# Performance work log

Measured on AMD Instinct MI355X. Metric: run time of the kernel, lower is better.

The kernel has to match this reference:

```python
import jax, jax.numpy as jnp
import numpy as np

N = 16384          # tokens
D_IN = 512         # input_dim
D_OUT = 512        # output_dim
H = 256            # expert hidden
E = 10             # num_experts
TOP_K = 2


def setup_inputs() -> dict:
    key = jax.random.key(0)
    ks = jax.random.split(key, 12)
    s_in = 1.0 / np.sqrt(D_IN)
    s_h = 1.0 / np.sqrt(H)
    s_o = 1.0 / np.sqrt(D_OUT)
    return {
        "x": jax.random.normal(ks[0], (N, D_IN), dtype=jnp.float32),
        "gate_w": jax.random.uniform(ks[1], (D_IN, E), minval=-s_in, maxval=s_in),
        "gate_b": jax.random.uniform(ks[2], (E,), minval=-s_in, maxval=s_in),
        "w1": jax.random.uniform(ks[3], (E, D_IN, H), minval=-s_in, maxval=s_in),
        "b1": jax.random.uniform(ks[4], (E, H), minval=-s_in, maxval=s_in),
        "w2": jax.random.uniform(ks[5], (E, H, D_OUT), minval=-s_h, maxval=s_h),
        "b2": jax.random.uniform(ks[6], (E, D_OUT), minval=-s_h, maxval=s_h),
        "cls_w": jax.random.uniform(ks[7], (D_OUT, D_OUT), minval=-s_o, maxval=s_o),
        "cls_b": jax.random.uniform(ks[8], (D_OUT,), minval=-s_o, maxval=s_o),
        "vec_w": jax.random.uniform(ks[9], (D_OUT, D_OUT), minval=-s_o, maxval=s_o),
        "vec_b": jax.random.uniform(ks[10], (D_OUT,), minval=-s_o, maxval=s_o),
    }


def reference(x, gate_w, gate_b, w1, b1, w2, b2, cls_w, cls_b, vec_w, vec_b):
    # Gating: softmax over experts, take top-k, renormalize
    gate_probs = jax.nn.softmax(x @ gate_w + gate_b, axis=-1)          # [N, E]
    top_v, top_i = jax.lax.top_k(gate_probs, TOP_K)                    # [N, K]
    top_v = top_v / jnp.sum(top_v, axis=-1, keepdims=True)
    # Scatter renormalized top-k probs into dense per-expert weights [N, E]
    n_idx = jnp.arange(x.shape[0])[:, None]
    w = jnp.zeros_like(gate_probs).at[n_idx, top_i].add(top_v)
    # Expert MLPs (vectorized over experts; zero weight == not dispatched)
    h = jax.nn.relu(jnp.einsum("nd,edh->neh", x, w1) + b1)             # [N, E, H]
    y = jnp.einsum("neh,eho->neo", h, w2) + b2                          # [N, E, Dout]
    combined = jnp.einsum("neo,ne->no", y, w)                           # [N, Dout]
    cls_out = combined @ cls_w + cls_b
    vec_out = combined @ vec_w + vec_b
    return (cls_out, vec_out)
```

## Files before the change

### kernel.cpp

```cpp
#include <hip/hip_runtime.h>

#define NTOK 16384
#define DIN  512
#define DOUT 512
#define HDIM 256
#define NEXP 10
#define NSLOT (2*NTOK)
#define NSEG  (2*NEXP)
#define BM 128
#define BN 128
#define BK 64

typedef unsigned short u16;
typedef unsigned int   u32;
typedef short s16x8 __attribute__((ext_vector_type(8)));
typedef float f32x4 __attribute__((ext_vector_type(4)));

__device__ __forceinline__ u16 f2b(float f){
  union { float f; u32 u; } c; c.f = f;
  u32 r = c.u + 0x7FFFu + ((c.u >> 16) & 1u);
  return (u16)(r >> 16);
}
__device__ __forceinline__ float b2f(u16 v){
  union { u32 u; float f; } c; c.u = ((u32)v) << 16; return c.f;
}
__device__ __forceinline__ u32 pk2(float lo, float hi){
  u32 r;
  asm("v_cvt_pk_bf16_f32 %0, %1, %2" : "=v"(r) : "v"(lo), "v"(hi));
  return r;
}
__device__ __forceinline__ s16x8 cvt8(const float* p){
  f32x4 a = *(const f32x4*)p;
  f32x4 b = *(const f32x4*)(p + 4);
  union { u32 u[4]; s16x8 v; } c;
  c.u[0] = pk2(a[0], a[1]); c.u[1] = pk2(a[2], a[3]);
  c.u[2] = pk2(b[0], b[1]); c.u[3] = pk2(b[2], b[3]);
  return c.v;
}

__global__ __launch_bounds__(64) void k_zero(int* counts){
  if (threadIdx.x < NSEG) counts[threadIdx.x] = 0;
}

__global__ __launch_bounds__(256) void k_gate(
    const float* __restrict__ x, const float* __restrict__ gw, const float* __restrict__ gb,
    int* __restrict__ tke, float* __restrict__ tkw, int* __restrict__ counts)
{
  __shared__ int cnt[NSEG];
  __shared__ __align__(16) float xs[16*512];
  __shared__ __align__(16) float lgw[5120];
  const int tid = threadIdx.x;
  if (tid < NSEG) cnt[tid] = 0;
  for (int d = tid; d < 512; d += 256){
    float g[10];
    #pragma unroll
    for (int r = 0; r < 10; ++r) g[r] = gw[d*10 + r];
    #pragma unroll
    for (int p = 0; p < 5; ++p){
      lgw[(p*512 + d)*2    ] = g[2*p];
      lgw[(p*512 + d)*2 + 1] = g[2*p+1];
    }
  }
  const float* xsrc = x + (size_t)blockIdx.x * 16 * 512;
  #pragma unroll
  for (int q = 0; q < 8; ++q){
    int i = tid + q*256;
    *(f32x4*)&xs[i*4] = *(const f32x4*)&xsrc[i*4];
  }
  __syncthreads();

  const int wave = tid >> 6, lane = tid & 63;
  #pragma unroll
  for (int tt = 0; tt < 4; ++tt){
    const int lt = wave*4 + tt;
    const int token = blockIdx.x*16 + lt;
    float acc[NEXP];
    #pragma unroll
    for (int e = 0; e < NEXP; ++e) acc[e] = 0.f;
    #pragma unroll
    for (int dd = 0; dd < 8; ++dd){
      int d = dd*64 + lane;
      float xv = xs[lt*512 + d];
      #pragma unroll
      for (int p = 0; p < 5; ++p){
        float2 g2 = *(const float2*)&lgw[(p*512 + d)*2];
        acc[2*p]   += xv * g2.x;
        acc[2*p+1] += xv * g2.y;
      }
    }
    #pragma unroll
    for (int e = 0; e < NEXP; ++e){
      #pragma unroll
      for (int off = 32; off > 0; off >>= 1) acc[e] += __shfl_xor(acc[e], off, 64);
    }
    if (lane == 0){
      float l[NEXP];
      #pragma unroll
      for (int e = 0; e < NEXP; ++e) l[e] = acc[e] + gb[e];
      int bi = 0; float bv = l[0];
      #pragma unroll
      for (int e = 1; e < NEXP; ++e) if (l[e] > bv){ bv = l[e]; bi = e; }
      int si = -1; float sv = -1e30f;
      #pragma unroll
      for (int e = 0; e < NEXP; ++e) if (e != bi && l[e] > sv){ sv = l[e]; si = e; }
      float w0 = 1.f / (1.f + expf(sv - bv));
      tke[2*token]   = bi;  tke[2*token+1] = si;
      tkw[2*token]   = w0;  tkw[2*token+1] = 1.f - w0;
      atomicAdd(&cnt[2*bi], 1);  atomicAdd(&cnt[2*si+1], 1);
    }
  }
  __syncthreads();
  if (tid < NSEG && cnt[tid] > 0)
    atomicAdd(&counts[tid], cnt[tid]);
}

__global__ __launch_bounds__(64) void k_scan(
    const int* __restrict__ counts, int* __restrict__ offsets, int* __restrict__ cursors)
{
  if (threadIdx.x == 0){
    int s = 0;
    for (int i = 0; i < NSEG; ++i){ offsets[i] = s; s += counts[i]; }
    offsets[NSEG] = s;
  }
  if (threadIdx.x < NSEG) cursors[threadIdx.x] = 0;
}

__global__ __launch_bounds__(256) void k_scatter(
    const int* __restrict__ tke, const float* __restrict__ tkw,
    const int* __restrict__ offsets, int* __restrict__ cursors,
    int* __restrict__ tok_slot, float* __restrict__ w_slot)
{
  __shared__ int lcnt[NSEG], lbase[NSEG];
  if (threadIdx.x < NSEG) lcnt[threadIdx.x] = 0;
  __syncthreads();
  int n = blockIdx.x * 256 + threadIdx.x;
  int g0 = 2*tke[2*n], g1 = 2*tke[2*n+1] + 1;
  int p0 = atomicAdd(&lcnt[g0], 1);
  int p1 = atomicAdd(&lcnt[g1], 1);
  __syncthreads();
  if (threadIdx.x < NSEG) lbase[threadIdx.x] = atomicAdd(&cursors[threadIdx.x], lcnt[threadIdx.x]);
  __syncthreads();
  int s0 = offsets[g0] + lbase[g0] + p0;
  int s1 = offsets[g1] + lbase[g1] + p1;
  tok_slot[s0] = n; w_slot[s0] = tkw[2*n];
  tok_slot[s1] = n; w_slot[s1] = tkw[2*n+1];
}

__global__ __launch_bounds__(256) void k_wtf(
    const float* __restrict__ W, u16* __restrict__ out, int KC8, int C16)
{
  const int e   = blockIdx.z;
  const int gid = blockIdx.x * 256 + threadIdx.x;
  const int c16 = gid & 15;
  const int rem = gid >> 4;
  const int kc  = rem % KC8;
  const int cg  = rem / KC8;
  const int K = KC8 * 8, C = C16 * 16;
  const float* src = W + (size_t)e*K*C + (size_t)(kc*8)*C + cg*16 + c16;
  s16x8 v;
  #pragma unroll
  for (int q = 0; q < 8; ++q)
    v[q] = (short)f2b(src[(size_t)q * C]);
  size_t t = ((size_t)e*C16 + cg)*KC8 + kc;
  *(s16x8*)(out + t*128 + c16*8) = v;
}

__global__ __launch_bounds__(256, 3) void k_h(
    const float* __restrict__ x, const u16* __restrict__ w1f, const float* __restrict__ b1,
    const int* __restrict__ offsets, const int* __restrict__ tok_slot,
    u16* __restrict__ h)
{
  __shared__ __align__(16) char pool[34816];
  u16* As = (u16*)pool;
  __shared__ int toks[BM];
  const int e   = blockIdx.z;
  const int hh  = blockIdx.y;
  const int off = offsets[2*e];
  const int cnt = offsets[2*e+2] - off;
  const int c0  = blockIdx.x * BM;
  if (c0 >= cnt) return;
  const int tid = threadIdx.x;

  if (tid < BM){
    int r = c0 + tid;
    toks[tid] = tok_slot[off + (r < cnt ? r : cnt - 1)];
  }
  __syncthreads();

  int crow[4], ckk[4];
  #pragma unroll
  for (int i = 0; i < 4; ++i){
    int c = tid + i*256;
    crow[i] = c >> 3; ckk[i] = (c & 7) * 8;
  }
  int tokr[4];
  #pragma unroll
  for (int i = 0; i < 4; ++i) tokr[i] = toks[crow[i]];

  s16x8 ra[4];
  auto loadregs = [&](int ks){
    #pragma unroll
    for (int i = 0; i < 4; ++i)
      ra[i] = cvt8(x + (size_t)tokr[i]*DIN + ks*BK + ckk[i]);
  };
  auto writeregs = [&](int buf){
    #pragma unroll
    for (int i = 0; i < 4; ++i){
      u32 byt = (u32)((crow[i]*BK + ckk[i])*2) ^ ((u32)(crow[i]&7)<<4);
      *(s16x8*)((char*)As + buf*16384 + byt) = ra[i];
    }
  };

  const int wv = tid >> 6, lane = tid & 63;
  const int lr = lane & 15, lk = lane >> 4;
  const int wr = (wv >> 1) * 64, wc = (wv & 1) * 64;
  const int cgb = e*16 + hh*8 + (wv & 1)*4;

  f32x4 acc[4][4];
  #pragma unroll
  for (int i = 0; i < 4; ++i)
    #pragma unroll
    for (int j = 0; j < 4; ++j) acc[i][j] = (f32x4){0.f,0.f,0.f,0.f};

  loadregs(0); writeregs(0);
  int cur = 0;
  const int NK = DIN / BK;
  for (int ks = 0; ks < NK; ++ks){
    __syncthreads();
    if (ks + 1 < NK) loadregs(ks + 1);
    #pragma unroll
    for (int sub = 0; sub < 2; ++sub){
      int kc = ks*8 + sub*4 + lk;
      s16x8 af[4], bf[4];
      #pragma unroll
      for (int g = 0; g < 4; ++g){
        int arow = wr + g*16 + lr;
        u32 ab = (u32)((arow*BK + sub*32 + lk*8)*2) ^ ((u32)(arow&7)<<4);
        af[g] = *(const s16x8*)((char*)As + cur*16384 + ab);
        bf[g] = *(const s16x8*)(w1f + ((size_t)(cgb + g)*64 + kc)*128 + lr*8);
      }
      #pragma unroll
      for (int i = 0; i < 4; ++i)
        #pragma unroll
        for (int j = 0; j < 4; ++j)
          acc[i][j] = __builtin_amdgcn_mfma_f32_16x16x32_bf16(af[i], bf[j], acc[i][j], 0, 0, 0);
    }
    if (ks + 1 < NK) writeregs(cur ^ 1);
    cur ^= 1;
  }
  __syncthreads();

  u16* outh = (u16*)pool;
  const int n0 = hh * 128;
  #pragma unroll
  for (int j = 0; j < 4; ++j){
    int col = wc + j*16 + lr;
    float bias = b1[e*HDIM + n0 + col];
    #pragma unroll
    for (int i = 0; i < 4; ++i)
      #pragma unroll
      for (int r = 0; r < 4; ++r){
        int row = wr + i*16 + lk*4 + r;
        float v = acc[i][j][r] + bias;
        outh[row*136 + col] = f2b(v > 0.f ? v : 0.f);
      }
  }
  __syncthreads();
  {
    int r = tid >> 1, half = tid & 1;
    if (c0 + r < cnt){
      u16* dst = h + (size_t)(off + c0 + r) * HDIM + n0 + half*64;
      const u16* src = outh + r*136 + half*64;
      #pragma unroll
      for (int q = 0; q < 8; ++q)
        *(s16x8*)(dst + q*8) = *(const s16x8*)(src + q*8);
    }
  }
}

template<int PASS>
__global__ __launch_bounds__(256, 3) void k_y(
    const u16* __restrict__ h, const u16* __restrict__ w2f, const float* __restrict__ b2,
    const int* __restrict__ offsets, const int* __restrict__ tok_slot,
    const float* __restrict__ w_slot, u16* __restrict__ cmb)
{
  __shared__ __align__(16) char pool[34816];
  u16* As = (u16*)pool;
  __shared__ int   toks[BM];
  __shared__ float wts[BM];
  const int e    = blockIdx.z;
  const int q4   = blockIdx.y;
  const int segb = offsets[2*e + PASS];
  const int segc = offsets[2*e + PASS + 1] - segb;
  const int c0   = blockIdx.x * BM;
  if (c0 >= segc) return;
  const int n0   = q4 * BN;
  const int tid  = threadIdx.x;

  if (tid < BM){
    int r = c0 + tid;
    int s = segb + (r < segc ? r : segc - 1);
    toks[tid] = tok_slot[s];
    wts[tid]  = w_slot[s];
  }
  __syncthreads();

  const u16* Ag = h + (size_t)(segb + c0) * HDIM;

  int crow[4], ckk[4];
  #pragma unroll
  for (int i = 0; i < 4; ++i){
    int c = tid + i*256;
    crow[i] = c >> 3; ckk[i] = (c & 7) * 8;
  }
  s16x8 ra[4];
  auto loadregs = [&](int ks){
    #pragma unroll
    for (int i = 0; i < 4; ++i)
      ra[i] = *(const s16x8*)(Ag + (size_t)crow[i]*HDIM + ks*BK + ckk[i]);
  };
  auto writeregs = [&](int buf){
    #pragma unroll
    for (int i = 0; i < 4; ++i){
      u32 byt = (u32)((crow[i]*BK + ckk[i])*2) ^ ((u32)(crow[i]&7)<<4);
      *(s16x8*)((char*)As + buf*16384 + byt) = ra[i];
    }
  };

  const int wv = tid >> 6, lane = tid & 63;
  const int lr = lane & 15, lk = lane >> 4;
  const int wr = (wv >> 1) * 64, wc = (wv & 1) * 64;
  const int cgb = e*32 + q4*8 + (wv & 1)*4;

  f32x4 acc[4][4];
  #pragma unroll
  for (int i = 0; i < 4; ++i)
    #pragma unroll
    for (int j = 0; j < 4; ++j) acc[i][j] = (f32x4){0.f,0.f,0.f,0.f};

  loadregs(0); writeregs(0);
  int cur = 0;
  const int NK = HDIM / BK;
  for (int ks = 0; ks < NK; ++ks){
    __syncthreads();
    if (ks + 1 < NK) loadregs(ks + 1);
    #pragma unroll
    for (int sub = 0; sub < 2; ++sub){
      int kc = ks*8 + sub*4 + lk;
      s16x8 af[4], bf[4];
      #pragma unroll
      for (int g = 0; g < 4; ++g){
        int arow = wr + g*16 + lr;
        u32 ab = (u32)((arow*BK + sub*32 + lk*8)*2) ^ ((u32)(arow&7)<<4);
        af[g] = *(const s16x8*)((char*)As + cur*16384 + ab);
        bf[g] = *(const s16x8*)(w2f + ((size_t)(cgb + g)*32 + kc)*128 + lr*8);
      }
      #pragma unroll
      for (int i = 0; i < 4; ++i)
        #pragma unroll
        for (int j = 0; j < 4; ++j)
          acc[i][j] = __builtin_amdgcn_mfma_f32_16x16x32_bf16(af[i], bf[j], acc[i][j], 0, 0, 0);
    }
    if (ks + 1 < NK) writeregs(cur ^ 1);
    cur ^= 1;
  }
  __syncthreads();

  u16* outh = (u16*)pool;
  #pragma unroll
  for (int j = 0; j < 4; ++j){
    int col = wc + j*16 + lr;
    float bias = b2[e*DOUT + n0 + col];
    #pragma unroll
    for (int i = 0; i < 4; ++i)
      #pragma unroll
      for (int r = 0; r < 4; ++r){
        int row = wr + i*16 + lk*4 + r;
        outh[row*136 + col] = f2b(wts[row] * (acc[i][j][r] + bias));
      }
  }
  __syncthreads();
  {
    int r = tid >> 1, half = tid & 1;
    if (c0 + r < segc){
      u16* dst = cmb + (size_t)toks[r] * 1024 + n0 + half*64;
      const u16* src = outh + r*136 + half*64;
      #pragma unroll
      for (int q = 0; q < 8; ++q){
        s16x8 s = *(const s16x8*)(src + q*8);
        if (PASS == 1){
          s16x8 old = *(const s16x8*)(dst + q*8);
          #pragma unroll
          for (int m = 0; m < 8; ++m)
            s[m] = (short)f2b(b2f((u16)old[m]) + b2f((u16)s[m]));
        }
        *(s16x8*)(dst + q*8) = s;
      }
    }
  }
}

__global__ __launch_bounds__(512, 4) void k_cls(
    const u16* __restrict__ cmb, const float* __restrict__ W,
    const float* __restrict__ bias, float* __restrict__ out)
{
  __shared__ __align__(16) char Bs[2][10240];
  const int tid = threadIdx.x;
  const int r0  = blockIdx.x * 256;
  const int c0  = blockIdx.y * 128;

  const int bc4 = tid >> 4;
  const int bkp = tid & 15;
  u32 bpk[4];
  auto loadB = [&](int ks){
    const float* p0 = W + (size_t)(ks*32 + 2*bkp) * DOUT + c0 + bc4*4;
    f32x4 v0 = *(const f32x4*)p0;
    f32x4 v1 = *(const f32x4*)(p0 + DOUT);
    #pragma unroll
    for (int m = 0; m < 4; ++m) bpk[m] = pk2(v0[m], v1[m]);
  };
  auto writeB = [&](int buf){
    #pragma unroll
    for (int m = 0; m < 4; ++m)
      *(u32*)(Bs[buf] + (bc4*4 + m)*80 + bkp*4) = bpk[m];
  };

  const int wv = tid >> 6, lane = tid & 63;
  const int lr = lane & 15, lk = lane >> 4;
  const int rg = wv >> 1, cg = wv & 1;
  const u16* Arow = cmb + (size_t)(r0 + rg*64) * 1024;

  f32x4 acc[4][4];
  #pragma unroll
  for (int i = 0; i < 4; ++i)
    #pragma unroll
    for (int j = 0; j < 4; ++j) acc[i][j] = (f32x4){0.f,0.f,0.f,0.f};

  s16x8 af[4], afn[4];
  auto loadA = [&](s16x8* a, int ks){
    #pragma unroll
    for (int g = 0; g < 4; ++g)
      a[g] = *(const s16x8*)(Arow + (size_t)(g*16 + lr)*1024 + ks*32 + lk*8);
  };

  loadB(0); writeB(0); loadA(af, 0);
  int cur = 0;
  for (int ks = 0; ks < 16; ++ks){
    __syncthreads();
    if (ks + 1 < 16){ loadB(ks + 1); loadA(afn, ks + 1); }
    s16x8 bf[4];
    #pragma unroll
    for (int j = 0; j < 4; ++j)
      bf[j] = *(const s16x8*)(Bs[cur] + (cg*64 + j*16 + lr)*80 + lk*16);
    #pragma unroll
    for (int i = 0; i < 4; ++i)
      #pragma unroll
      for (int j = 0; j < 4; ++j)
        acc[i][j] = __builtin_amdgcn_mfma_f32_16x16x32_bf16(af[i], bf[j], acc[i][j], 0, 0, 0);
    if (ks + 1 < 16) writeB(cur ^ 1);
    #pragma unroll
    for (int g = 0; g < 4; ++g) af[g] = afn[g];
    cur ^= 1;
  }

  #pragma unroll
  for (int j = 0; j < 4; ++j){
    int col = c0 + cg*64 + j*16 + lr;
    float bv = bias[col];
    #pragma unroll
    for (int i = 0; i < 4; ++i)
      #pragma unroll
      for (int r = 0; r < 4; ++r){
        int row = r0 + rg*64 + i*16 + lk*4 + r;
        out[(size_t)row * DOUT + col] = acc[i][j][r] + bv;
      }
  }
}

__global__ __launch_bounds__(512, 2) void k_vip(
    const float* __restrict__ W, const float* __restrict__ bias,
    u16* __restrict__ cmbio)
{
  __shared__ __align__(16) char Bs[2][40960];
  const int tid = threadIdx.x;
  const int r0  = blockIdx.x * 64;

  int bc4[4], bkp[4];
  #pragma unroll
  for (int u = 0; u < 4; ++u){
    int idx = tid + u*512;
    bc4[u] = idx >> 4;
    bkp[u] = idx & 15;
  }
  u32 bpk[4][4];
  auto loadB = [&](int ks){
    #pragma unroll
    for (int u = 0; u < 4; ++u){
      const float* p0 = W + (size_t)(ks*32 + 2*bkp[u]) * DOUT + bc4[u]*4;
      f32x4 v0 = *(const f32x4*)p0;
      f32x4 v1 = *(const f32x4*)(p0 + DOUT);
      #pragma unroll
      for (int m = 0; m < 4; ++m) bpk[u][m] = pk2(v0[m], v1[m]);
    }
  };
  auto writeB = [&](int buf){
    #pragma unroll
    for (int u = 0; u < 4; ++u)
      #pragma unroll
      for (int m = 0; m < 4; ++m)
        *(u32*)(Bs[buf] + (bc4[u]*4 + m)*80 + bkp[u]*4) = bpk[u][m];
  };

  const int wv = tid >> 6, lane = tid & 63;
  const int lr = lane & 15, lk = lane >> 4;
  const int wc = wv * 64;
  const u16* Arow = cmbio + (size_t)r0 * 1024;

  f32x4 acc[4][4];
  #pragma unroll
  for (int i = 0; i < 4; ++i)
    #pragma unroll
    for (int j = 0; j < 4; ++j) acc[i][j] = (f32x4){0.f,0.f,0.f,0.f};

  s16x8 af[4], afn[4];
  auto loadA = [&](s16x8* a, int ks){
    #pragma unroll
    for (int g = 0; g < 4; ++g)
      a[g] = *(const s16x8*)(Arow + (size_t)(g*16 + lr)*1024 + ks*32 + lk*8);
  };

  loadB(0); writeB(0); loadA(af, 0);
  int cur = 0;
  for (int ks = 0; ks < 16; ++ks){
    __syncthreads();
    if (ks + 1 < 16){ loadB(ks + 1); loadA(afn, ks + 1); }
    s16x8 bf[4];
    #pragma unroll
    for (int g = 0; g < 4; ++g)
      bf[g] = *(const s16x8*)(Bs[cur] + (wc + g*16 + lr)*80 + lk*16);
    #pragma unroll
    for (int i = 0; i < 4; ++i)
      #pragma unroll
      for (int j = 0; j < 4; ++j)
        acc[i][j] = __builtin_amdgcn_mfma_f32_16x16x32_bf16(af[i], bf[j], acc[i][j], 0, 0, 0);
    if (ks + 1 < 16) writeB(cur ^ 1);
    #pragma unroll
    for (int g = 0; g < 4; ++g) af[g] = afn[g];
    cur ^= 1;
  }
  __syncthreads();

  float* out = (float*)cmbio;
  #pragma unroll
  for (int j = 0; j < 4; ++j){
    int col = wc + j*16 + lr;
    float bv = bias[col];
    #pragma unroll
    for (int i = 0; i < 4; ++i)
      #pragma unroll
      for (int r = 0; r < 4; ++r){
        int row = r0 + i*16 + lk*4 + r;
        out[(size_t)row * DOUT + col] = acc[i][j][r] + bv;
      }
  }
}

__global__ __launch_bounds__(256, 2) void k_vipw(
    const u16* __restrict__ wTt, const float* __restrict__ bias,
    u16* __restrict__ cmbio)
{
  const int tid = threadIdx.x;
  const int r0  = blockIdx.x * 32;
  const int wv = tid >> 6, lane = tid & 63;
  const int lr = lane & 15, lk = lane >> 4;
  const int wc = wv * 128;
  const int cg0 = wv * 8;
  const u16* Arow = cmbio + (size_t)r0 * 1024;

  f32x4 acc[2][8];
  #pragma unroll
  for (int i = 0; i < 2; ++i)
    #pragma unroll
    for (int j = 0; j < 8; ++j) acc[i][j] = (f32x4){0.f,0.f,0.f,0.f};

  s16x8 a0[2], b0[8], a1[2], b1[8];
  auto loadA = [&](s16x8* a, int ks){
    #pragma unroll
    for (int g = 0; g < 2; ++g)
      a[g] = *(const s16x8*)(Arow + (size_t)(g*16 + lr)*1024 + ks*32 + lk*8);
  };
  auto loadB = [&](s16x8* b, int ks){
    #pragma unroll
    for (int j = 0; j < 8; ++j){
      int chunk = (cg0 + j)*64 + ks*4 + lk;
      b[j] = *(const s16x8*)(wTt + (size_t)chunk*128 + lr*8);
    }
  };
  auto step = [&](const s16x8* a, const s16x8* b){
    #pragma unroll
    for (int j = 0; j < 8; ++j)
      #pragma unroll
      for (int i = 0; i < 2; ++i)
        acc[i][j] = __builtin_amdgcn_mfma_f32_16x16x32_bf16(a[i], b[j], acc[i][j], 0, 0, 0);
  };

  loadA(a0, 0); loadB(b0, 0);
  #pragma unroll
  for (int ks = 0; ks < 16; ks += 2){
    if (ks + 1 < 16){ loadA(a1, ks + 1); loadB(b1, ks + 1); }
    step(a0, b0);
    if (ks + 2 < 16){ loadA(a0, ks + 2); loadB(b0, ks + 2); }
    step(a1, b1);
  }
  __syncthreads();

  float* out = (float*)cmbio;
  #pragma unroll
  for (int j = 0; j < 8; ++j){
    int col = wc + j*16 + lr;
    float bv = bias[col];
    #pragma unroll
    for (int i = 0; i < 2; ++i)
      #pragma unroll
      for (int r = 0; r < 4; ++r){
        int row = r0 + i*16 + lk*4 + r;
        out[(size_t)row * DOUT + col] = acc[i][j][r] + bv;
      }
  }
}

extern "C" void kernel_launch(void* const* d_in, const int* in_sizes, int n_in,
                              void* d_out, int out_size, void* d_ws, size_t ws_size,
                              hipStream_t stream)
{
  const float* x    = (const float*)d_in[0];
  const float* gw   = (const float*)d_in[1];
  const float* gb   = (const float*)d_in[2];
  const float* w1   = (const float*)d_in[3];
  const float* b1   = (const float*)d_in[4];
  const float* w2   = (const float*)d_in[5];
  const float* b2   = (const float*)d_in[6];
  const float* clsw = (const float*)d_in[7];
  const float* clsb = (const float*)d_in[8];
  const float* vecw = (const float*)d_in[9];
  const float* vecb = (const float*)d_in[10];

  char* base = (char*)d_out;
  float* cls_out  = (float*)base;
  u16*   cmb      = (u16*)(base + ((size_t)32<<20));
  u16*   h        = (u16*)base;
  char*  mb       = base + ((size_t)16<<20) + (128<<10);
  int*   tok_slot = (int*)  mb;
  float* w_slot   = (float*)(mb + 131072);
  int*   tke      = (int*)  (mb + 262144);
  float* tkw      = (float*)(mb + 393216);
  int*   counts   = (int*)  (mb + 524288);
  int*   offsets  = (int*)  (mb + 524544);
  int*   cursors  = (int*)  (mb + 524800);
  u16*   w1f      = (u16*)(base + ((size_t)18<<20));
  u16*   w2f      = (u16*)(base + ((size_t)21<<20));

  const bool usews = (ws_size >= (size_t)(1<<20));
  u16* vecwTt = (u16*)d_ws;

  k_zero<<<dim3(1), dim3(64), 0, stream>>>(counts);
  k_gate<<<dim3(NTOK/16), dim3(256), 0, stream>>>(x, gw, gb, tke, tkw, counts);
  k_scan<<<dim3(1), dim3(64), 0, stream>>>(counts, offsets, cursors);
  k_scatter<<<dim3(NTOK/256), dim3(256), 0, stream>>>(tke, tkw, offsets, cursors,
                                                      tok_slot, w_slot);
  k_wtf<<<dim3(64, 1, NEXP), dim3(256), 0, stream>>>(w1, w1f, 64, 16);
  k_wtf<<<dim3(64, 1, NEXP), dim3(256), 0, stream>>>(w2, w2f, 32, 32);
  if (usews)
    k_wtf<<<dim3(128, 1, 1), dim3(256), 0, stream>>>(vecw, vecwTt, 64, 32);
  k_h<<<dim3(256, 2, NEXP), dim3(256), 0, stream>>>(x, w1f, b1, offsets, tok_slot, h);
  k_y<0><<<dim3(128, 4, NEXP), dim3(256), 0, stream>>>(h, w2f, b2, offsets, tok_slot, w_slot, cmb);
  k_y<1><<<dim3(128, 4, NEXP), dim3(256), 0, stream>>>(h, w2f, b2, offsets, tok_slot, w_slot, cmb);
  k_cls<<<dim3(NTOK/256, DOUT/128), dim3(512), 0, stream>>>(cmb, clsw, clsb, cls_out);
  if (usews)
    k_vipw<<<dim3(NTOK/32), dim3(256), 0, stream>>>(vecwTt, vecb, cmb);
  else
    k_vip<<<dim3(NTOK/64), dim3(512), 0, stream>>>(vecw, vecb, cmb);
}
```

Measured before the change: 203.7 us.

## Fuse expert up-projection and down-projection into one kernel keeping hidden in LDS

Replaces the separate k_h (x·W1 + relu to global h) and k_y (h·W2) kernels with a fused k_ey that computes a 64-token tile's hidden activations into shared memory and immediately multiplies by W2 for all 512 outputs. This removes the global round trip of the bf16 hidden buffer and one kernel launch. In exchange, each block now reads full W1 and W2 slices per 64 rows, and the fused kernel is run once per slot pass, so the up-projection on x is split across two launches. Both passes now recompute the gather and conversion of x. B operands still come straight from global memory, and each wave holds only one 16-row A fragment, which lowers MFMA reuse.

```diff
diff --git a/kernel.cpp b/kernel.cpp
--- a/kernel.cpp
+++ b/kernel.cpp
@@ -7,9 +7,6 @@
 #define NEXP 10
 #define NSLOT (2*NTOK)
 #define NSEG  (2*NEXP)
-#define BM 128
-#define BN 128
-#define BK 64
 
 typedef unsigned short u16;
 typedef unsigned int   u32;
@@ -165,139 +162,27 @@
   *(s16x8*)(out + t*128 + c16*8) = v;
 }
 
-__global__ __launch_bounds__(256, 3) void k_h(
-    const float* __restrict__ x, const u16* __restrict__ w1f, const float* __restrict__ b1,
-    const int* __restrict__ offsets, const int* __restrict__ tok_slot,
-    u16* __restrict__ h)
-{
-  __shared__ __align__(16) char pool[34816];
-  u16* As = (u16*)pool;
-  __shared__ int toks[BM];
-  const int e   = blockIdx.z;
-  const int hh  = blockIdx.y;
-  const int off = offsets[2*e];
-  const int cnt = offsets[2*e+2] - off;
-  const int c0  = blockIdx.x * BM;
-  if (c0 >= cnt) return;
-  const int tid = threadIdx.x;
-
-  if (tid < BM){
-    int r = c0 + tid;
-    toks[tid] = tok_slot[off + (r < cnt ? r : cnt - 1)];
-  }
-  __syncthreads();
-
-  int crow[4], ckk[4];
-  #pragma unroll
-  for (int i = 0; i < 4; ++i){
-    int c = tid + i*256;
-    crow[i] = c >> 3; ckk[i] = (c & 7) * 8;
-  }
-  int tokr[4];
-  #pragma unroll
-  for (int i = 0; i < 4; ++i) tokr[i] = toks[crow[i]];
-
-  s16x8 ra[4];
-  auto loadregs = [&](int ks){
-    #pragma unroll
-    for (int i = 0; i < 4; ++i)
-      ra[i] = cvt8(x + (size_t)tokr[i]*DIN + ks*BK + ckk[i]);
-  };
-  auto writeregs = [&](int buf){
-    #pragma unroll
-    for (int i = 0; i < 4; ++i){
-      u32 byt = (u32)((crow[i]*BK + ckk[i])*2) ^ ((u32)(crow[i]&7)<<4);
-      *(s16x8*)((char*)As + buf*16384 + byt) = ra[i];
-    }
-  };
-
-  const int wv = tid >> 6, lane = tid & 63;
-  const int lr = lane & 15, lk = lane >> 4;
-  const int wr = (wv >> 1) * 64, wc = (wv & 1) * 64;
-  const int cgb = e*16 + hh*8 + (wv & 1)*4;
-
-  f32x4 acc[4][4];
-  #pragma unroll
-  for (int i = 0; i < 4; ++i)
-    #pragma unroll
-    for (int j = 0; j < 4; ++j) acc[i][j] = (f32x4){0.f,0.f,0.f,0.f};
-
-  loadregs(0); writeregs(0);
-  int cur = 0;
-  const int NK = DIN / BK;
-  for (int ks = 0; ks < NK; ++ks){
-    __syncthreads();
-    if (ks + 1 < NK) loadregs(ks + 1);
-    #pragma unroll
-    for (int sub = 0; sub < 2; ++sub){
-      int kc = ks*8 + sub*4 + lk;
-      s16x8 af[4], bf[4];
-      #pragma unroll
-      for (int g = 0; g < 4; ++g){
-        int arow = wr + g*16 + lr;
-        u32 ab = (u32)((arow*BK + sub*32 + lk*8)*2) ^ ((u32)(arow&7)<<4);
-        af[g] = *(const s16x8*)((char*)As + cur*16384 + ab);
-        bf[g] = *(const s16x8*)(w1f + ((size_t)(cgb + g)*64 + kc)*128 + lr*8);
-      }
-      #pragma unroll
-      for (int i = 0; i < 4; ++i)
-        #pragma unroll
-        for (int j = 0; j < 4; ++j)
-          acc[i][j] = __builtin_amdgcn_mfma_f32_16x16x32_bf16(af[i], bf[j], acc[i][j], 0, 0, 0);
-    }
-    if (ks + 1 < NK) writeregs(cur ^ 1);
-    cur ^= 1;
-  }
-  __syncthreads();
-
-  u16* outh = (u16*)pool;
-  const int n0 = hh * 128;
-  #pragma unroll
-  for (int j = 0; j < 4; ++j){
-    int col = wc + j*16 + lr;
-    float bias = b1[e*HDIM + n0 + col];
-    #pragma unroll
-    for (int i = 0; i < 4; ++i)
-      #pragma unroll
-      for (int r = 0; r < 4; ++r){
-        int row = wr + i*16 + lk*4 + r;
-        float v = acc[i][j][r] + bias;
-        outh[row*136 + col] = f2b(v > 0.f ? v : 0.f);
-      }
-  }
-  __syncthreads();
-  {
-    int r = tid >> 1, half = tid & 1;
-    if (c0 + r < cnt){
-      u16* dst = h + (size_t)(off + c0 + r) * HDIM + n0 + half*64;
-      const u16* src = outh + r*136 + half*64;
-      #pragma unroll
-      for (int q = 0; q < 8; ++q)
-        *(s16x8*)(dst + q*8) = *(const s16x8*)(src + q*8);
-    }
-  }
-}
-
 template<int PASS>
-__global__ __launch_bounds__(256, 3) void k_y(
-    const u16* __restrict__ h, const u16* __restrict__ w2f, const float* __restrict__ b2,
+__global__ __launch_bounds__(512, 4) void k_ey(
+    const float* __restrict__ x,
+    const u16* __restrict__ w1f, const float* __restrict__ b1,
+    const u16* __restrict__ w2f, const float* __restrict__ b2,
     const int* __restrict__ offsets, const int* __restrict__ tok_slot,
     const float* __restrict__ w_slot, u16* __restrict__ cmb)
 {
-  __shared__ __align__(16) char pool[34816];
-  u16* As = (u16*)pool;
-  __shared__ int   toks[BM];
-  __shared__ float wts[BM];
+  __shared__ __align__(16) char pool[50176];
+  u16* As   = (u16*)pool;
+  u16* hbuf = (u16*)(pool + 16384);
+  __shared__ int   toks[64];
+  __shared__ float wts[64];
   const int e    = blockIdx.z;
-  const int q4   = blockIdx.y;
   const int segb = offsets[2*e + PASS];
   const int segc = offsets[2*e + PASS + 1] - segb;
-  const int c0   = blockIdx.x * BM;
+  const int c0   = blockIdx.x * 64;
   if (c0 >= segc) return;
-  const int n0   = q4 * BN;
   const int tid  = threadIdx.x;
 
-  if (tid < BM){
+  if (tid < 64){
     int r = c0 + tid;
     int s = segb + (r < segc ? r : segc - 1);
     toks[tid] = tok_slot[s];
@@ -305,98 +190,113 @@
   }
   __syncthreads();
 
-  const u16* Ag = h + (size_t)(segb + c0) * HDIM;
-
-  int crow[4], ckk[4];
-  #pragma unroll
-  for (int i = 0; i < 4; ++i){
-    int c = tid + i*256;
-    crow[i] = c >> 3; ckk[i] = (c & 7) * 8;
-  }
-  s16x8 ra[4];
+  const int crow = tid >> 3;
+  const int ckk  = (tid & 7) * 8;
+  const int tokr = toks[crow];
+
+  s16x8 ra;
   auto loadregs = [&](int ks){
-    #pragma unroll
-    for (int i = 0; i < 4; ++i)
-      ra[i] = *(const s16x8*)(Ag + (size_t)crow[i]*HDIM + ks*BK + ckk[i]);
+    ra = cvt8(x + (size_t)tokr*DIN + ks*64 + ckk);
   };
   auto writeregs = [&](int buf){
-    #pragma unroll
-    for (int i = 0; i < 4; ++i){
-      u32 byt = (u32)((crow[i]*BK + ckk[i])*2) ^ ((u32)(crow[i]&7)<<4);
-      *(s16x8*)((char*)As + buf*16384 + byt) = ra[i];
-    }
+    u32 byt = (u32)((crow*64 + ckk)*2) ^ ((u32)(crow&7)<<4);
+    *(s16x8*)((char*)As + buf*8192 + byt) = ra;
   };
 
   const int wv = tid >> 6, lane = tid & 63;
   const int lr = lane & 15, lk = lane >> 4;
-  const int wr = (wv >> 1) * 64, wc = (wv & 1) * 64;
-  const int cgb = e*32 + q4*8 + (wv & 1)*4;
-
-  f32x4 acc[4][4];
-  #pragma unroll
-  for (int i = 0; i < 4; ++i)
-    #pragma unroll
-    for (int j = 0; j < 4; ++j) acc[i][j] = (f32x4){0.f,0.f,0.f,0.f};
+  const int wr = (wv >> 1) * 16;
+  const int ch = wv & 1;
+
+  f32x4 acc1[8];
+  #pragma unroll
+  for (int j = 0; j < 8; ++j) acc1[j] = (f32x4){0.f,0.f,0.f,0.f};
+  const int cgb1 = e*16 + ch*8;
 
   loadregs(0); writeregs(0);
   int cur = 0;
-  const int NK = HDIM / BK;
-  for (int ks = 0; ks < NK; ++ks){
+  for (int ks = 0; ks < 8; ++ks){
     __syncthreads();
-    if (ks + 1 < NK) loadregs(ks + 1);
+    if (ks + 1 < 8) loadregs(ks + 1);
     #pragma unroll
     for (int sub = 0; sub < 2; ++sub){
       int kc = ks*8 + sub*4 + lk;
-      s16x8 af[4], bf[4];
-      #pragma unroll
-      for (int g = 0; g < 4; ++g){
-        int arow = wr + g*16 + lr;
-        u32 ab = (u32)((arow*BK + sub*32 + lk*8)*2) ^ ((u32)(arow&7)<<4);
-        af[g] = *(const s16x8*)((char*)As + cur*16384 + ab);
-        bf[g] = *(const s16x8*)(w2f + ((size_t)(cgb + g)*32 + kc)*128 + lr*8);
-      }
-      #pragma unroll
-      for (int i = 0; i < 4; ++i)
+      int arow = wr + lr;
+      u32 ab = (u32)((arow*64 + sub*32 + lk*8)*2) ^ ((u32)(arow&7)<<4);
+      s16x8 af = *(const s16x8*)((char*)As + cur*8192 + ab);
+      #pragma unroll
+      for (int g = 0; g < 8; ++g){
+        s16x8 bf = *(const s16x8*)(w1f + ((size_t)(cgb1 + g)*64 + kc)*128 + lr*8);
+        acc1[g] = __builtin_amdgcn_mfma_f32_16x16x32_bf16(af, bf, acc1[g], 0, 0, 0);
+      }
+    }
+    if (ks + 1 < 8) writeregs(cur ^ 1);
+    cur ^= 1;
+  }
+  #pragma unroll
+  for (int g = 0; g < 8; ++g){
+    int col = ch*128 + g*16 + lr;
+    float bias = b1[e*HDIM + col];
+    #pragma unroll
+    for (int r = 0; r < 4; ++r){
+      int row = wr + lk*4 + r;
+      float v = acc1[g][r] + bias;
+      hbuf[row*264 + col] = f2b(v > 0.f ? v : 0.f);
+    }
+  }
+  __syncthreads();
+
+  f32x4 acc2[16];
+  #pragma unroll
+  for (int g = 0; g < 16; ++g) acc2[g] = (f32x4){0.f,0.f,0.f,0.f};
+  const int cgb2 = e*32 + ch*16;
+
+  for (int kk = 0; kk < 8; ++kk){
+    s16x8 af = *(const s16x8*)&hbuf[(wr + lr)*264 + kk*32 + lk*8];
+    int kc = kk*4 + lk;
+    #pragma unroll
+    for (int g = 0; g < 16; ++g){
+      s16x8 bf = *(const s16x8*)(w2f + ((size_t)(cgb2 + g)*32 + kc)*128 + lr*8);
+      acc2[g] = __builtin_amdgcn_mfma_f32_16x16x32_bf16(af, bf, acc2[g], 0, 0, 0);
+    }
+  }
+  __syncthreads();
+
+  u16* stage = (u16*)pool;
+  #pragma unroll
+  for (int cc = 0; cc < 2; ++cc){
+    if (ch == cc){
+      #pragma unroll
+      for (int g = 0; g < 16; ++g){
+        int col = g*16 + lr;
+        float bias = b2[e*DOUT + cc*256 + col];
         #pragma unroll
-        for (int j = 0; j < 4; ++j)
-          acc[i][j] = __builtin_amdgcn_mfma_f32_16x16x32_bf16(af[i], bf[j], acc[i][j], 0, 0, 0);
-    }
-    if (ks + 1 < NK) writeregs(cur ^ 1);
-    cur ^= 1;
-  }
-  __syncthreads();
-
-  u16* outh = (u16*)pool;
-  #pragma unroll
-  for (int j = 0; j < 4; ++j){
-    int col = wc + j*16 + lr;
-    float bias = b2[e*DOUT + n0 + col];
-    #pragma unroll
-    for (int i = 0; i < 4; ++i)
-      #pragma unroll
-      for (int r = 0; r < 4; ++r){
-        int row = wr + i*16 + lk*4 + r;
-        outh[row*136 + col] = f2b(wts[row] * (acc[i][j][r] + bias));
-      }
-  }
-  __syncthreads();
-  {
-    int r = tid >> 1, half = tid & 1;
-    if (c0 + r < segc){
-      u16* dst = cmb + (size_t)toks[r] * 1024 + n0 + half*64;
-      const u16* src = outh + r*136 + half*64;
-      #pragma unroll
-      for (int q = 0; q < 8; ++q){
-        s16x8 s = *(const s16x8*)(src + q*8);
-        if (PASS == 1){
-          s16x8 old = *(const s16x8*)(dst + q*8);
-          #pragma unroll
-          for (int m = 0; m < 8; ++m)
-            s[m] = (short)f2b(b2f((u16)old[m]) + b2f((u16)s[m]));
+        for (int r = 0; r < 4; ++r){
+          int row = wr + lk*4 + r;
+          stage[row*264 + col] = f2b(wts[row] * (acc2[g][r] + bias));
         }
-        *(s16x8*)(dst + q*8) = s;
-      }
-    }
+      }
+    }
+    __syncthreads();
+    {
+      int row = tid >> 3, t8 = tid & 7;
+      if (c0 + row < segc){
+        u16* dst = cmb + (size_t)toks[row] * 1024 + cc*256 + t8*32;
+        const u16* src = stage + row*264 + t8*32;
+        #pragma unroll
+        for (int q = 0; q < 4; ++q){
+          s16x8 s = *(const s16x8*)(src + q*8);
+          if (PASS == 1){
+            s16x8 old = *(const s16x8*)(dst + q*8);
+            #pragma unroll
+            for (int m = 0; m < 8; ++m)
+              s[m] = (short)f2b(b2f((u16)old[m]) + b2f((u16)s[m]));
+          }
+          *(s16x8*)(dst + q*8) = s;
+        }
+      }
+    }
+    __syncthreads();
   }
 }
 
@@ -648,7 +548,6 @@
   char* base = (char*)d_out;
   float* cls_out  = (float*)base;
   u16*   cmb      = (u16*)(base + ((size_t)32<<20));
-  u16*   h        = (u16*)base;
   char*  mb       = base + ((size_t)16<<20) + (128<<10);
   int*   tok_slot = (int*)  mb;
   float* w_slot   = (float*)(mb + 131072);
@@ -672,9 +571,10 @@
   k_wtf<<<dim3(64, 1, NEXP), dim3(256), 0, stream>>>(w2, w2f, 32, 32);
   if (usews)
     k_wtf<<<dim3(128, 1, 1), dim3(256), 0, stream>>>(vecw, vecwTt, 64, 32);
-  k_h<<<dim3(256, 2, NEXP), dim3(256), 0, stream>>>(x, w1f, b1, offsets, tok_slot, h);
-  k_y<0><<<dim3(128, 4, NEXP), dim3(256), 0, stream>>>(h, w2f, b2, offsets, tok_slot, w_slot, cmb);
-  k_y<1><<<dim3(128, 4, NEXP), dim3(256), 0, stream>>>(h, w2f, b2, offsets, tok_slot, w_slot, cmb);
+  k_ey<0><<<dim3(256, 1, NEXP), dim3(512), 0, stream>>>(x, w1f, b1, w2f, b2,
+                                                        offsets, tok_slot, w_slot, cmb);
+  k_ey<1><<<dim3(256, 1, NEXP), dim3(512), 0, stream>>>(x, w1f, b1, w2f, b2,
+                                                        offsets, tok_slot, w_slot, cmb);
   k_cls<<<dim3(NTOK/256, DOUT/128), dim3(512), 0, stream>>>(cmb, clsw, clsb, cls_out);
   if (usews)
     k_vipw<<<dim3(NTOK/32), dim3(256), 0, stream>>>(vecwTt, vecb, cmb);
```

After: 283.0 us. 38.9% more time.

## Pre-pack cls weights to bf16 fragments and drop LDS staging in cls GEMM

Applied to the files above, without the earlier changes.

Adds a kernel that converts cls_w to bf16 in MFMA fragment order and stores it in the otherwise unused upper half of the first rows of the combined buffer. The classifier GEMM is rewritten so each block handles 32 rows across all 512 output columns, reading pre-packed B fragments straight from global memory with register double-buffering instead of converting fp32 weights into shared memory with barriers each k-step. This removes per-block weight conversion and LDS syncs, but relies on the spare region of cmb staying untouched until k_cls2 runs, and it leans on cache for the B reloads.

```diff
diff --git a/kernel.cpp b/kernel.cpp
--- a/kernel.cpp
+++ b/kernel.cpp
@@ -163,6 +163,24 @@
     v[q] = (short)f2b(src[(size_t)q * C]);
   size_t t = ((size_t)e*C16 + cg)*KC8 + kc;
   *(s16x8*)(out + t*128 + c16*8) = v;
+}
+
+__global__ __launch_bounds__(256) void k_wtc(
+    const float* __restrict__ W, u16* __restrict__ cmb)
+{
+  const int gid = blockIdx.x * 256 + threadIdx.x;
+  const int c16 = gid & 15;
+  const int rem = gid >> 4;
+  const int kc  = rem % 64;
+  const int cg  = rem / 64;
+  const float* src = W + (size_t)(kc*8)*DOUT + cg*16 + c16;
+  s16x8 v;
+  #pragma unroll
+  for (int q = 0; q < 8; ++q)
+    v[q] = (short)f2b(src[(size_t)q * DOUT]);
+  size_t t = (size_t)cg*64 + kc;
+  u16* dst = cmb + (t>>2)*1024 + 512 + (t&3)*128 + c16*8;
+  *(s16x8*)dst = v;
 }
 
 __global__ __launch_bounds__(256, 3) void k_h(
@@ -400,78 +418,63 @@
   }
 }
 
-__global__ __launch_bounds__(512, 4) void k_cls(
-    const u16* __restrict__ cmb, const float* __restrict__ W,
-    const float* __restrict__ bias, float* __restrict__ out)
-{
-  __shared__ __align__(16) char Bs[2][10240];
+__global__ __launch_bounds__(256, 2) void k_cls2(
+    const u16* __restrict__ cmb, const float* __restrict__ bias,
+    float* __restrict__ out)
+{
   const int tid = threadIdx.x;
-  const int r0  = blockIdx.x * 256;
-  const int c0  = blockIdx.y * 128;
-
-  const int bc4 = tid >> 4;
-  const int bkp = tid & 15;
-  u32 bpk[4];
-  auto loadB = [&](int ks){
-    const float* p0 = W + (size_t)(ks*32 + 2*bkp) * DOUT + c0 + bc4*4;
-    f32x4 v0 = *(const f32x4*)p0;
-    f32x4 v1 = *(const f32x4*)(p0 + DOUT);
-    #pragma unroll
-    for (int m = 0; m < 4; ++m) bpk[m] = pk2(v0[m], v1[m]);
-  };
-  auto writeB = [&](int buf){
-    #pragma unroll
-    for (int m = 0; m < 4; ++m)
-      *(u32*)(Bs[buf] + (bc4*4 + m)*80 + bkp*4) = bpk[m];
-  };
-
+  const int r0  = blockIdx.x * 32;
   const int wv = tid >> 6, lane = tid & 63;
   const int lr = lane & 15, lk = lane >> 4;
-  const int rg = wv >> 1, cg = wv & 1;
-  const u16* Arow = cmb + (size_t)(r0 + rg*64) * 1024;
-
-  f32x4 acc[4][4];
-  #pragma unroll
-  for (int i = 0; i < 4; ++i)
-    #pragma unroll
-    for (int j = 0; j < 4; ++j) acc[i][j] = (f32x4){0.f,0.f,0.f,0.f};
-
-  s16x8 af[4], afn[4];
+  const int wc = wv * 128;
+  const int cg0 = wv * 8;
+  const u16* Arow = cmb + (size_t)r0 * 1024;
+
+  f32x4 acc[2][8];
+  #pragma unroll
+  for (int i = 0; i < 2; ++i)
+    #pragma unroll
+    for (int j = 0; j < 8; ++j) acc[i][j] = (f32x4){0.f,0.f,0.f,0.f};
+
+  s16x8 a0[2], b0[8], a1[2], b1[8];
   auto loadA = [&](s16x8* a, int ks){
     #pragma unroll
-    for (int g = 0; g < 4; ++g)
+    for (int g = 0; g < 2; ++g)
       a[g] = *(const s16x8*)(Arow + (size_t)(g*16 + lr)*1024 + ks*32 + lk*8);
   };
-
-  loadB(0); writeB(0); loadA(af, 0);
-  int cur = 0;
-  for (int ks = 0; ks < 16; ++ks){
-    __syncthreads();
-    if (ks + 1 < 16){ loadB(ks + 1); loadA(afn, ks + 1); }
-    s16x8 bf[4];
-    #pragma unroll
-    for (int j = 0; j < 4; ++j)
-      bf[j] = *(const s16x8*)(Bs[cur] + (cg*64 + j*16 + lr)*80 + lk*16);
-    #pragma unroll
-    for (int i = 0; i < 4; ++i)
-      #pragma unroll
-      for (int j = 0; j < 4; ++j)
-        acc[i][j] = __builtin_amdgcn_mfma_f32_16x16x32_bf16(af[i], bf[j], acc[i][j], 0, 0, 0);
-    if (ks + 1 < 16) writeB(cur ^ 1);
-    #pragma unroll
-    for (int g = 0; g < 4; ++g) af[g] = afn[g];
-    cur ^= 1;
-  }
-
-  #pragma unroll
-  for (int j = 0; j < 4; ++j){
-    int col = c0 + cg*64 + j*16 + lr;
+  auto loadB = [&](s16x8* b, int ks){
+    #pragma unroll
+    for (int j = 0; j < 8; ++j){
+      int chunk = (cg0 + j)*64 + ks*4 + lk;
+      b[j] = *(const s16x8*)(cmb + (size_t)(chunk>>2)*1024 + 512 + (chunk&3)*128 + lr*8);
+    }
+  };
+  auto step = [&](const s16x8* a, const s16x8* b){
+    #pragma unroll
+    for (int j = 0; j < 8; ++j)
+      #pragma unroll
+      for (int i = 0; i < 2; ++i)
+        acc[i][j] = __builtin_amdgcn_mfma_f32_16x16x32_bf16(a[i], b[j], acc[i][j], 0, 0, 0);
+  };
+
+  loadA(a0, 0); loadB(b0, 0);
+  #pragma unroll
+  for (int ks = 0; ks < 16; ks += 2){
+    if (ks + 1 < 16){ loadA(a1, ks + 1); loadB(b1, ks + 1); }
+    step(a0, b0);
+    if (ks + 2 < 16){ loadA(a0, ks + 2); loadB(b0, ks + 2); }
+    step(a1, b1);
+  }
+
+  #pragma unroll
+  for (int j = 0; j < 8; ++j){
+    int col = wc + j*16 + lr;
     float bv = bias[col];
     #pragma unroll
-    for (int i = 0; i < 4; ++i)
+    for (int i = 0; i < 2; ++i)
       #pragma unroll
       for (int r = 0; r < 4; ++r){
-        int row = r0 + rg*64 + i*16 + lk*4 + r;
+        int row = r0 + i*16 + lk*4 + r;
         out[(size_t)row * DOUT + col] = acc[i][j][r] + bv;
       }
   }
@@ -670,12 +673,13 @@
                                                       tok_slot, w_slot);
   k_wtf<<<dim3(64, 1, NEXP), dim3(256), 0, stream>>>(w1, w1f, 64, 16);
   k_wtf<<<dim3(64, 1, NEXP), dim3(256), 0, stream>>>(w2, w2f, 32, 32);
+  k_wtc<<<dim3(128), dim3(256), 0, stream>>>(clsw, cmb);
   if (usews)
     k_wtf<<<dim3(128, 1, 1), dim3(256), 0, stream>>>(vecw, vecwTt, 64, 32);
   k_h<<<dim3(256, 2, NEXP), dim3(256), 0, stream>>>(x, w1f, b1, offsets, tok_slot, h);
   k_y<0><<<dim3(128, 4, NEXP), dim3(256), 0, stream>>>(h, w2f, b2, offsets, tok_slot, w_slot, cmb);
   k_y<1><<<dim3(128, 4, NEXP), dim3(256), 0, stream>>>(h, w2f, b2, offsets, tok_slot, w_slot, cmb);
-  k_cls<<<dim3(NTOK/256, DOUT/128), dim3(512), 0, stream>>>(cmb, clsw, clsb, cls_out);
+  k_cls2<<<dim3(NTOK/32), dim3(256), 0, stream>>>(cmb, clsb, cls_out);
   if (usews)
     k_vipw<<<dim3(NTOK/32), dim3(256), 0, stream>>>(vecwTt, vecb, cmb);
   else
```

New measurement: 214.0 us. 5.1% more time.
